# Optimization experiments

Measured on AMD Instinct MI355X. Metric: run time of the kernel, lower is better.

The kernel has to match this reference:

```python
import jax, jax.numpy as jnp
import numpy as np

N_NODES = 4096
D_MODEL = 1024
MAX_DEPS = 8
N_CLASSES = 64


def setup_inputs() -> dict:
    key = jax.random.key(0)
    k1, k2, k3 = jax.random.split(key, 3)
    questions = jax.random.normal(k1, (N_NODES, D_MODEL), dtype=jnp.float32)
    # Padded dependency lists; every dependency index is strictly < node index,
    # so processing nodes in index order is a valid topological order.
    rng = np.random.default_rng(0)
    dep_idx = np.zeros((N_NODES, MAX_DEPS), dtype=np.int32)
    dep_mask = np.zeros((N_NODES, MAX_DEPS), dtype=np.int32)
    for i in range(1, N_NODES):
        nd = int(rng.integers(1, MAX_DEPS + 1))
        dep_idx[i, :nd] = rng.integers(0, i, size=nd)
        dep_mask[i, :nd] = 1
    W1 = jax.random.normal(k2, (D_MODEL, 2 * D_MODEL), dtype=jnp.float32) * 0.02
    b1 = jnp.zeros((D_MODEL,), dtype=jnp.float32)
    W2 = jax.random.normal(k3, (N_CLASSES, D_MODEL), dtype=jnp.float32) * 0.02
    b2 = jnp.zeros((N_CLASSES,), dtype=jnp.float32)
    return {
        "questions": questions,
        "W1": W1,
        "b1": b1,
        "W2": W2,
        "b2": b2,
        "dep_idx": jnp.asarray(dep_idx),
        "dep_mask": jnp.asarray(dep_mask),
    }


def reference(questions, W1, b1, W2, b2, dep_idx, dep_mask):
    n_nodes, d_model = questions.shape

    def step(answers, xs):
        i, q, deps, mask = xs
        ctx = answers[deps]                       # [MAX_DEPS, d_model] gather
        m = mask.astype(q.dtype)
        # masked mean; all-zero mask -> zero context (matches torch zeros branch)
        ctx_mean = (ctx * m[:, None]).sum(0) / jnp.maximum(m.sum(), 1.0)
        combined = jnp.concatenate([q, ctx_mean])  # [2*d_model]
        h = jax.nn.gelu(combined @ W1.T + b1, approximate=False)
        return answers.at[i].set(h), None

    answers0 = jnp.zeros((n_nodes, d_model), dtype=questions.dtype)
    xs = (jnp.arange(n_nodes), questions, dep_idx, dep_mask)
    answers, _ = jax.lax.scan(step, answers0, xs)
    root_answer = answers[n_nodes - 1]            # root = last node in topo order
    return root_answer @ W2.T + b2                # [n_classes] logits
```

## Files before the change

kernel.cpp:

```cpp
#include <hip/hip_runtime.h>

#define NN 4096
#define DM 1024
#define MD 8
#define NW 256
#define NCOL 4
#define NT 512
#define NWAVE (NT / 64)
#define UR 4
#define MAXL 4097

#define MI_NLEV 0
#define MI_ROOTPOS 1
#define MI_ARRIVE 8
#define MI_LO 1024
#define MI_NL 6144
#define MI_PERM 10240
#define MI_DCNT 14336
#define MI_INV 18432
#define MI_DPOS 22528

typedef __attribute__((ext_vector_type(8))) short bf16x8;
typedef __attribute__((ext_vector_type(8))) unsigned short ushort8;
typedef __attribute__((ext_vector_type(4))) float f32x4;

__device__ __forceinline__ float gelu_f(float x) {
  return 0.5f * x * (1.0f + erff(x * 0.70710678118654752440f));
}
__device__ __forceinline__ unsigned short f2bf(float x) {
  unsigned int u = __builtin_bit_cast(unsigned int, x);
  u += 0x7FFFu + ((u >> 16) & 1u);
  return (unsigned short)(u >> 16);
}
__device__ __forceinline__ float bf2f(unsigned short v) {
  return __builtin_bit_cast(float, (unsigned int)v << 16);
}

__global__ __launch_bounds__(1024) void k_cvt(
    const float* __restrict__ Q, unsigned short* __restrict__ Qb) {
  const int t = threadIdx.x;
  const size_t total = (size_t)NN * DM / 8;
  for (size_t c = (size_t)blockIdx.x * 1024 + t; c < total; c += 255 * 1024) {
    const size_t i = c * 8;
    float4 a = *(const float4*)&Q[i];
    float4 b = *(const float4*)&Q[i + 4];
    ushort8 o;
    o[0] = f2bf(a.x); o[1] = f2bf(a.y); o[2] = f2bf(a.z); o[3] = f2bf(a.w);
    o[4] = f2bf(b.x); o[5] = f2bf(b.y); o[6] = f2bf(b.z); o[7] = f2bf(b.w);
    *(ushort8*)&Qb[i] = o;
  }
}

__global__ __launch_bounds__(1024) void k_fused(
    const unsigned short* __restrict__ Qb, const float* __restrict__ W1,
    const float* __restrict__ b1, const int* __restrict__ dep_idx,
    const int* __restrict__ dep_mask, int* __restrict__ meta,
    float* __restrict__ preQ) {
  __shared__ int lvl[NN];
  __shared__ int liv[NN];
  __shared__ int cnt[2 * NN];
  __shared__ int pos[NN];
  __shared__ int wflag[2][16];
  __shared__ int s_max;
  const int t = threadIdx.x;

  if (blockIdx.x != 0) {
    if (t >= 256) return;
    const int bid = blockIdx.x - 1;
    const int wave = t >> 6, lane = t & 63;
    const int wm = wave >> 1, wn = wave & 1;
    const int m0 = (bid >> 3) * 128 + wm * 64;
    const int n0 = (bid & 7) * 128 + wn * 64;
    const int lrow = lane & 15;
    const int klo = (lane >> 4) * 8;
    f32x4 acc[4][4] = {};
    for (int k0 = 0; k0 < DM; k0 += 32) {
      bf16x8 af[4];
      #pragma unroll
      for (int f = 0; f < 4; ++f)
        af[f] = *(const bf16x8*)&Qb[(size_t)(m0 + f * 16 + lrow) * DM + k0 + klo];
      bf16x8 bfr[4];
      #pragma unroll
      for (int g = 0; g < 4; ++g) {
        const float* wsrc = &W1[(size_t)(n0 + g * 16 + lrow) * 2048 + k0 + klo];
        float4 w0 = *(const float4*)&wsrc[0];
        float4 w1 = *(const float4*)&wsrc[4];
        bf16x8 bb;
        bb[0] = (short)f2bf(w0.x); bb[1] = (short)f2bf(w0.y);
        bb[2] = (short)f2bf(w0.z); bb[3] = (short)f2bf(w0.w);
        bb[4] = (short)f2bf(w1.x); bb[5] = (short)f2bf(w1.y);
        bb[6] = (short)f2bf(w1.z); bb[7] = (short)f2bf(w1.w);
        bfr[g] = bb;
      }
      #pragma unroll
      for (int f = 0; f < 4; ++f)
        #pragma unroll
        for (int g = 0; g < 4; ++g)
          acc[f][g] = __builtin_amdgcn_mfma_f32_16x16x32_bf16(af[f], bfr[g], acc[f][g], 0, 0, 0);
    }
    float b1v[4];
    #pragma unroll
    for (int g = 0; g < 4; ++g) b1v[g] = b1[n0 + g * 16 + lrow];
    const int mrow = (lane >> 4) * 4;
    #pragma unroll
    for (int f = 0; f < 4; ++f)
      #pragma unroll
      for (int g = 0; g < 4; ++g) {
        const int n = n0 + g * 16 + lrow;
        #pragma unroll
        for (int r = 0; r < 4; ++r)
          preQ[(size_t)(m0 + f * 16 + mrow + r) * DM + n] = acc[f][g][r] + b1v[g];
      }
    return;
  }

  for (int i = t; i < NN; i += 1024) { lvl[i] = 0; liv[i] = (i == NN - 1) ? 1 : 0; }
  for (int i = t; i < 2 * NN; i += 1024) cnt[i] = 0;
  if (t == 0) s_max = 0;
  __syncthreads();

  const int wid = t >> 6;
  int par = 0;

  for (int u = 0; u < 4; ++u) {
    const int i = u * 1024 + t;
    const int4 d0 = *(const int4*)&dep_idx[i * MD];
    const int4 d1 = *(const int4*)&dep_idx[i * MD + 4];
    const int4 m0 = *(const int4*)&dep_mask[i * MD];
    const int4 m1 = *(const int4*)&dep_mask[i * MD + 4];
    int my = 0;
    for (;;) {
      int m = 0;
      if (m0.x) { int l = lvl[d0.x] + 1; m = m > l ? m : l; }
      if (m0.y) { int l = lvl[d0.y] + 1; m = m > l ? m : l; }
      if (m0.z) { int l = lvl[d0.z] + 1; m = m > l ? m : l; }
      if (m0.w) { int l = lvl[d0.w] + 1; m = m > l ? m : l; }
      if (m1.x) { int l = lvl[d1.x] + 1; m = m > l ? m : l; }
      if (m1.y) { int l = lvl[d1.y] + 1; m = m > l ? m : l; }
      if (m1.z) { int l = lvl[d1.z] + 1; m = m > l ? m : l; }
      if (m1.w) { int l = lvl[d1.w] + 1; m = m > l ? m : l; }
      bool ch = false;
      if (m > my) { my = m; lvl[i] = m; ch = true; }
      const bool anyw = (__ballot(ch) != 0);
      if ((t & 63) == 0) wflag[par][wid] = anyw ? 1 : 0;
      __syncthreads();
      int any = 0;
      #pragma unroll
      for (int w = 0; w < 16; ++w) any |= wflag[par][w];
      par ^= 1;
      if (!any) break;
    }
  }
  for (int u = 3; u >= 0; --u) {
    const int i = u * 1024 + t;
    const int4 d0 = *(const int4*)&dep_idx[i * MD];
    const int4 d1 = *(const int4*)&dep_idx[i * MD + 4];
    const int4 m0 = *(const int4*)&dep_mask[i * MD];
    const int4 m1 = *(const int4*)&dep_mask[i * MD + 4];
    for (;;) {
      bool ch = false;
      if (liv[i]) {
        if (m0.x && !liv[d0.x]) { liv[d0.x] = 1; ch = true; }
        if (m0.y && !liv[d0.y]) { liv[d0.y] = 1; ch = true; }
        if (m0.z && !liv[d0.z]) { liv[d0.z] = 1; ch = true; }
        if (m0.w && !liv[d0.w]) { liv[d0.w] = 1; ch = true; }
        if (m1.x && !liv[d1.x]) { liv[d1.x] = 1; ch = true; }
        if (m1.y && !liv[d1.y]) { liv[d1.y] = 1; ch = true; }
        if (m1.z && !liv[d1.z]) { liv[d1.z] = 1; ch = true; }
        if (m1.w && !liv[d1.w]) { liv[d1.w] = 1; ch = true; }
      }
      const bool anyw = (__ballot(ch) != 0);
      if ((t & 63) == 0) wflag[par][wid] = anyw ? 1 : 0;
      __syncthreads();
      int any = 0;
      #pragma unroll
      for (int w = 0; w < 16; ++w) any |= wflag[par][w];
      par ^= 1;
      if (!any) break;
    }
  }
  for (int i = t; i < NN; i += 1024) {
    atomicAdd(&cnt[2 * lvl[i] + (liv[i] ? 0 : 1)], 1);
    atomicMax(&s_max, lvl[i]);
  }
  __syncthreads();
  const int nL = s_max + 1;
  if (t == 0) {
    int off = 0;
    for (int l = 0; l < nL; ++l) {
      meta[MI_LO + l] = off;
      meta[MI_NL + l] = cnt[2 * l];
      const int a = cnt[2 * l], b = cnt[2 * l + 1];
      cnt[2 * l] = off; off += a;
      cnt[2 * l + 1] = off; off += b;
    }
    meta[MI_LO + nL] = off;
    meta[MI_NLEV] = nL;
  }
  __syncthreads();
  for (int i = t; i < NN; i += 1024)
    pos[i] = atomicAdd(&cnt[2 * lvl[i] + (liv[i] ? 0 : 1)], 1);
  __syncthreads();
  for (int i = t; i < NN; i += 1024) {
    const int r = pos[i];
    meta[MI_PERM + r] = i;
    const int4 d0 = *(const int4*)&dep_idx[i * MD];
    const int4 d1 = *(const int4*)&dep_idx[i * MD + 4];
    const int4 m0 = *(const int4*)&dep_mask[i * MD];
    const int4 m1 = *(const int4*)&dep_mask[i * MD + 4];
    const int dd[8] = {d0.x, d0.y, d0.z, d0.w, d1.x, d1.y, d1.z, d1.w};
    const int mm[8] = {m0.x, m0.y, m0.z, m0.w, m1.x, m1.y, m1.z, m1.w};
    int nd = 0;
    #pragma unroll
    for (int k = 0; k < MD; ++k)
      if (mm[k]) { meta[MI_DPOS + r * MD + nd] = pos[dd[k]]; ++nd; }
    for (int k = nd; k < MD; ++k) meta[MI_DPOS + r * MD + k] = 0;
    meta[MI_DCNT + r] = nd;
    ((float*)meta)[MI_INV + r] = nd ? 1.0f / (float)nd : 0.0f;
  }
  if (t == 0) meta[MI_ROOTPOS] = pos[NN - 1];
  for (int i = t; i < NW; i += 1024) meta[MI_ARRIVE + i] = 0;
}

__global__ __launch_bounds__(NT) void k_levels(
    const float* __restrict__ W1, const float* __restrict__ preQ,
    unsigned short* __restrict__ hPb, float4* __restrict__ gPan, int* __restrict__ meta,
    const float* __restrict__ W2, const float* __restrict__ b2, float* __restrict__ out) {
  const int tid = threadIdx.x;
  const int wb = blockIdx.x;
  const int c0 = wb * NCOL;
  const int wave = tid >> 6, lane = tid & 63;
  const int nL = meta[MI_NLEV];
  const int rootRow = meta[MI_ROOTPOS];
  __shared__ int s_lo[MAXL];
  __shared__ int s_nl[MAXL];
  __shared__ float4 preLDS[NT];
  for (int i = tid; i <= nL; i += NT) s_lo[i] = meta[MI_LO + i];
  for (int i = tid; i < nL; i += NT) s_nl[i] = meta[MI_NL + i];
  float4 wreg[NCOL][4];
  #pragma unroll
  for (int cc = 0; cc < NCOL; ++cc)
    #pragma unroll
    for (int q = 0; q < 4; ++q)
      wreg[cc][q] = *(const float4*)&W1[(size_t)(c0 + cc) * 2048 + 1024 + lane * 16 + q * 4];
  __syncthreads();
  float4* gp = gPan + (size_t)wb * NN;
  const float* invA = (const float*)&meta[MI_INV];

  for (int l = 0; l < nL; ++l) {
    const int lo = s_lo[l];
    const int nA = s_nl[l];

    for (int r = lo + tid; r < lo + nA; r += NT) {
      const int node = meta[MI_PERM + r];
      const int nd = meta[MI_DCNT + r];
      const float iv = invA[r];
      const int4 p0 = *(const int4*)&meta[MI_DPOS + r * MD];
      const int4 p1 = *(const int4*)&meta[MI_DPOS + r * MD + 4];
      const int dps[8] = {p0.x, p0.y, p0.z, p0.w, p1.x, p1.y, p1.z, p1.w};
      float sx = 0.f, sy = 0.f, sz = 0.f, sw = 0.f;
      #pragma unroll
      for (int d = 0; d < MD; ++d) {
        float4 v = gp[dps[d]];
        sx += (d < nd) ? v.x : 0.f;
        sy += (d < nd) ? v.y : 0.f;
        sz += (d < nd) ? v.z : 0.f;
        sw += (d < nd) ? v.w : 0.f;
      }
      const float4 pq = (l > 0 && r == lo + tid) ? preLDS[tid]
                                                 : *(const float4*)&preQ[(size_t)node * DM + c0];
      const unsigned short h0 = f2bf(gelu_f(pq.x + sx * iv));
      const unsigned short h1 = f2bf(gelu_f(pq.y + sy * iv));
      const unsigned short h2 = f2bf(gelu_f(pq.z + sz * iv));
      const unsigned short h3 = f2bf(gelu_f(pq.w + sw * iv));
      const unsigned long long u = (unsigned long long)h0 | ((unsigned long long)h1 << 16)
                                 | ((unsigned long long)h2 << 32) | ((unsigned long long)h3 << 48);
      __hip_atomic_store((unsigned long long*)&hPb[(size_t)r * DM + c0], u,
                         __ATOMIC_RELAXED, __HIP_MEMORY_SCOPE_AGENT);
    }
    __syncthreads();
    if (tid == 0)
      __hip_atomic_store(&meta[MI_ARRIVE + wb], l + 1, __ATOMIC_RELAXED, __HIP_MEMORY_SCOPE_AGENT);
    if (l + 1 < nL && tid < s_nl[l + 1]) {
      const int node2 = meta[MI_PERM + s_lo[l + 1] + tid];
      preLDS[tid] = *(const float4*)&preQ[(size_t)node2 * DM + c0];
    }
    if (tid < 64) {
      for (;;) {
        int m = 1 << 30;
        #pragma unroll
        for (int u = 0; u < 4; ++u) {
          int v = __hip_atomic_load(&meta[MI_ARRIVE + tid * 4 + u], __ATOMIC_RELAXED, __HIP_MEMORY_SCOPE_AGENT);
          m = v < m ? v : m;
        }
        #pragma unroll
        for (int off = 1; off < 64; off <<= 1) {
          int o = __shfl_xor(m, off);
          m = o < m ? o : m;
        }
        if (m >= l + 1) break;
        __builtin_amdgcn_s_sleep(1);
      }
    }
    __syncthreads();

    for (int base = wave * UR; base < nA; base += NWAVE * UR) {
      const int cnt = nA - base;
      ushort8 hv[UR][2];
      #pragma unroll
      for (int u = 0; u < UR; ++u) {
        const int r = lo + base + ((u < cnt) ? u : 0);
        const ushort8* h8 = (const ushort8*)&hPb[(size_t)r * DM];
        hv[u][0] = h8[lane * 2];
        hv[u][1] = h8[lane * 2 + 1];
      }
      float rr[UR][NCOL];
      #pragma unroll
      for (int u = 0; u < UR; ++u) {
        float hf[16];
        #pragma unroll
        for (int e = 0; e < 8; ++e) { hf[e] = bf2f(hv[u][0][e]); hf[8 + e] = bf2f(hv[u][1][e]); }
        #pragma unroll
        for (int cc = 0; cc < NCOL; ++cc) {
          float a = 0.f;
          #pragma unroll
          for (int q = 0; q < 4; ++q)
            a += hf[q * 4 + 0] * wreg[cc][q].x + hf[q * 4 + 1] * wreg[cc][q].y
               + hf[q * 4 + 2] * wreg[cc][q].z + hf[q * 4 + 3] * wreg[cc][q].w;
          rr[u][cc] = a;
        }
      }
      #pragma unroll
      for (int off = 1; off < 64; off <<= 1)
        #pragma unroll
        for (int u = 0; u < UR; ++u)
          #pragma unroll
          for (int cc = 0; cc < NCOL; ++cc)
            rr[u][cc] += __shfl_xor(rr[u][cc], off);
      if (lane == 0) {
        #pragma unroll
        for (int u = 0; u < UR; ++u)
          if (u < cnt) gp[lo + base + u] = make_float4(rr[u][0], rr[u][1], rr[u][2], rr[u][3]);
      }
    }
    __syncthreads();
  }

  if (wb == 0) {
    float* red = (float*)preLDS;
    const int j = tid >> 3, kc = tid & 7;
    const ushort8* h8 = (const ushort8*)&hPb[(size_t)rootRow * DM];
    const float* wr2 = W2 + (size_t)j * DM;
    float acc = 0.f;
    for (int k = kc * 128; k < kc * 128 + 128; k += 8) {
      ushort8 hv = h8[k >> 3];
      float4 wa = *(const float4*)&wr2[k];
      float4 wb4 = *(const float4*)&wr2[k + 4];
      acc += bf2f(hv[0]) * wa.x + bf2f(hv[1]) * wa.y + bf2f(hv[2]) * wa.z + bf2f(hv[3]) * wa.w
           + bf2f(hv[4]) * wb4.x + bf2f(hv[5]) * wb4.y + bf2f(hv[6]) * wb4.z + bf2f(hv[7]) * wb4.w;
    }
    red[tid] = acc;
    __syncthreads();
    if (kc == 0) {
      float s = 0.f;
      #pragma unroll
      for (int e = 0; e < 8; ++e) s += red[j * 8 + e];
      out[j] = s + b2[j];
    }
  }
}

extern "C" void kernel_launch(void* const* d_in, const int* in_sizes, int n_in,
                              void* d_out, int out_size, void* d_ws, size_t ws_size,
                              hipStream_t stream) {
  const float* Q        = (const float*)d_in[0];
  const float* W1       = (const float*)d_in[1];
  const float* b1       = (const float*)d_in[2];
  const float* W2       = (const float*)d_in[3];
  const float* b2       = (const float*)d_in[4];
  const int*   dep_idx  = (const int*)d_in[5];
  const int*   dep_mask = (const int*)d_in[6];

  char* ws = (char*)d_ws;
  float*          preQ = (float*)ws;
  unsigned short* hPb  = (unsigned short*)(ws + (16ull << 20));
  unsigned short* Qb   = (unsigned short*)(ws + (24ull << 20));
  float4*         gPan = (float4*)(ws + (32ull << 20));
  int*            meta = (int*)(ws + (48ull << 20));
  float*          out  = (float*)d_out;

  k_cvt<<<dim3(255), dim3(1024), 0, stream>>>(Q, Qb);
  k_fused<<<dim3(257), dim3(1024), 0, stream>>>(Qb, W1, b1, dep_idx, dep_mask, meta, preQ);
  k_levels<<<dim3(NW), dim3(NT), 0, stream>>>(W1, preQ, hPb, gPan, meta, W2, b2, out);
}
```

Baseline: 481.7 us.

## Fuse question bf16 conversion into GEMM and run liveness pass in a separate block

```diff
diff --git a/kernel.cpp b/kernel.cpp
--- a/kernel.cpp
+++ b/kernel.cpp
@@ -12,6 +12,7 @@
 
 #define MI_NLEV 0
 #define MI_ROOTPOS 1
+#define MI_BWFLAG 2
 #define MI_ARRIVE 8
 #define MI_LO 1024
 #define MI_NL 6144
@@ -19,6 +20,7 @@
 #define MI_DCNT 14336
 #define MI_INV 18432
 #define MI_DPOS 22528
+#define MI_LIV 55296
 
 typedef __attribute__((ext_vector_type(8))) short bf16x8;
 typedef __attribute__((ext_vector_type(8))) unsigned short ushort8;
@@ -36,37 +38,23 @@
   return __builtin_bit_cast(float, (unsigned int)v << 16);
 }
 
-__global__ __launch_bounds__(1024) void k_cvt(
-    const float* __restrict__ Q, unsigned short* __restrict__ Qb) {
-  const int t = threadIdx.x;
-  const size_t total = (size_t)NN * DM / 8;
-  for (size_t c = (size_t)blockIdx.x * 1024 + t; c < total; c += 255 * 1024) {
-    const size_t i = c * 8;
-    float4 a = *(const float4*)&Q[i];
-    float4 b = *(const float4*)&Q[i + 4];
-    ushort8 o;
-    o[0] = f2bf(a.x); o[1] = f2bf(a.y); o[2] = f2bf(a.z); o[3] = f2bf(a.w);
-    o[4] = f2bf(b.x); o[5] = f2bf(b.y); o[6] = f2bf(b.z); o[7] = f2bf(b.w);
-    *(ushort8*)&Qb[i] = o;
-  }
-}
-
 __global__ __launch_bounds__(1024) void k_fused(
-    const unsigned short* __restrict__ Qb, const float* __restrict__ W1,
+    const float* __restrict__ Q, const float* __restrict__ W1,
     const float* __restrict__ b1, const int* __restrict__ dep_idx,
     const int* __restrict__ dep_mask, int* __restrict__ meta,
     float* __restrict__ preQ) {
   __shared__ int lvl[NN];
-  __shared__ int liv[NN];
-  __shared__ int cnt[2 * NN];
+  __shared__ int livS[NN];
+  __shared__ int cnt[2048];
   __shared__ int pos[NN];
   __shared__ int wflag[2][16];
   __shared__ int s_max;
   const int t = threadIdx.x;
-
-  if (blockIdx.x != 0) {
+  const int wid = t >> 6;
+
+  if (blockIdx.x >= 2) {
     if (t >= 256) return;
-    const int bid = blockIdx.x - 1;
+    const int bid = blockIdx.x - 2;
     const int wave = t >> 6, lane = t & 63;
     const int wm = wave >> 1, wn = wave & 1;
     const int m0 = (bid >> 3) * 128 + wm * 64;
@@ -77,8 +65,17 @@
     for (int k0 = 0; k0 < DM; k0 += 32) {
       bf16x8 af[4];
       #pragma unroll
-      for (int f = 0; f < 4; ++f)
-        af[f] = *(const bf16x8*)&Qb[(size_t)(m0 + f * 16 + lrow) * DM + k0 + klo];
+      for (int f = 0; f < 4; ++f) {
+        const float* qsrc = &Q[(size_t)(m0 + f * 16 + lrow) * DM + k0 + klo];
+        float4 q0 = *(const float4*)&qsrc[0];
+        float4 q1 = *(const float4*)&qsrc[4];
+        bf16x8 aa;
+        aa[0] = (short)f2bf(q0.x); aa[1] = (short)f2bf(q0.y);
+        aa[2] = (short)f2bf(q0.z); aa[3] = (short)f2bf(q0.w);
+        aa[4] = (short)f2bf(q1.x); aa[5] = (short)f2bf(q1.y);
+        aa[6] = (short)f2bf(q1.z); aa[7] = (short)f2bf(q1.w);
+        af[f] = aa;
+      }
       bf16x8 bfr[4];
       #pragma unroll
       for (int g = 0; g < 4; ++g) {
@@ -114,14 +111,52 @@
     return;
   }
 
-  for (int i = t; i < NN; i += 1024) { lvl[i] = 0; liv[i] = (i == NN - 1) ? 1 : 0; }
-  for (int i = t; i < 2 * NN; i += 1024) cnt[i] = 0;
+  if (blockIdx.x == 1) {
+    for (int i = t; i < NN; i += 1024) livS[i] = (i == NN - 1) ? 1 : 0;
+    __syncthreads();
+    int par = 0;
+    for (int u = 3; u >= 0; --u) {
+      const int i = u * 1024 + t;
+      const int4 d0 = *(const int4*)&dep_idx[i * MD];
+      const int4 d1 = *(const int4*)&dep_idx[i * MD + 4];
+      const int4 m0 = *(const int4*)&dep_mask[i * MD];
+      const int4 m1 = *(const int4*)&dep_mask[i * MD + 4];
+      for (;;) {
+        bool ch = false;
+        if (livS[i]) {
+          if (m0.x && !livS[d0.x]) { livS[d0.x] = 1; ch = true; }
+          if (m0.y && !livS[d0.y]) { livS[d0.y] = 1; ch = true; }
+          if (m0.z && !livS[d0.z]) { livS[d0.z] = 1; ch = true; }
+          if (m0.w && !livS[d0.w]) { livS[d0.w] = 1; ch = true; }
+          if (m1.x && !livS[d1.x]) { livS[d1.x] = 1; ch = true; }
+          if (m1.y && !livS[d1.y]) { livS[d1.y] = 1; ch = true; }
+          if (m1.z && !livS[d1.z]) { livS[d1.z] = 1; ch = true; }
+          if (m1.w && !livS[d1.w]) { livS[d1.w] = 1; ch = true; }
+        }
+        const bool anyw = (__ballot(ch) != 0);
+        if ((t & 63) == 0) wflag[par][wid] = anyw ? 1 : 0;
+        __syncthreads();
+        int any = 0;
+        #pragma unroll
+        for (int w = 0; w < 16; ++w) any |= wflag[par][w];
+        par ^= 1;
+        if (!any) break;
+      }
+    }
+    for (int i = t; i < NN; i += 1024)
+      __hip_atomic_store(&meta[MI_LIV + i], livS[i], __ATOMIC_RELAXED, __HIP_MEMORY_SCOPE_AGENT);
+    __syncthreads();
+    if (t == 0)
+      __hip_atomic_store(&meta[MI_BWFLAG], 1, __ATOMIC_RELAXED, __HIP_MEMORY_SCOPE_AGENT);
+    return;
+  }
+
+  for (int i = t; i < NN; i += 1024) lvl[i] = 0;
+  for (int i = t; i < 2048; i += 1024) cnt[i] = 0;
   if (t == 0) s_max = 0;
   __syncthreads();
 
-  const int wid = t >> 6;
   int par = 0;
-
   for (int u = 0; u < 4; ++u) {
     const int i = u * 1024 + t;
     const int4 d0 = *(const int4*)&dep_idx[i * MD];
@@ -151,36 +186,18 @@
       if (!any) break;
     }
   }
-  for (int u = 3; u >= 0; --u) {
-    const int i = u * 1024 + t;
-    const int4 d0 = *(const int4*)&dep_idx[i * MD];
-    const int4 d1 = *(const int4*)&dep_idx[i * MD + 4];
-    const int4 m0 = *(const int4*)&dep_mask[i * MD];
-    const int4 m1 = *(const int4*)&dep_mask[i * MD + 4];
-    for (;;) {
-      bool ch = false;
-      if (liv[i]) {
-        if (m0.x && !liv[d0.x]) { liv[d0.x] = 1; ch = true; }
-        if (m0.y && !liv[d0.y]) { liv[d0.y] = 1; ch = true; }
-        if (m0.z && !liv[d0.z]) { liv[d0.z] = 1; ch = true; }
-        if (m0.w && !liv[d0.w]) { liv[d0.w] = 1; ch = true; }
-        if (m1.x && !liv[d1.x]) { liv[d1.x] = 1; ch = true; }
-        if (m1.y && !liv[d1.y]) { liv[d1.y] = 1; ch = true; }
-        if (m1.z && !liv[d1.z]) { liv[d1.z] = 1; ch = true; }
-        if (m1.w && !liv[d1.w]) { liv[d1.w] = 1; ch = true; }
-      }
-      const bool anyw = (__ballot(ch) != 0);
-      if ((t & 63) == 0) wflag[par][wid] = anyw ? 1 : 0;
-      __syncthreads();
-      int any = 0;
-      #pragma unroll
-      for (int w = 0; w < 16; ++w) any |= wflag[par][w];
-      par ^= 1;
-      if (!any) break;
-    }
-  }
+
+  if (t == 0) {
+    while (__hip_atomic_load(&meta[MI_BWFLAG], __ATOMIC_RELAXED, __HIP_MEMORY_SCOPE_AGENT) != 1)
+      __builtin_amdgcn_s_sleep(8);
+  }
+  __syncthreads();
+  for (int i = t; i < NN; i += 1024)
+    livS[i] = __hip_atomic_load(&meta[MI_LIV + i], __ATOMIC_RELAXED, __HIP_MEMORY_SCOPE_AGENT);
+  __syncthreads();
+
   for (int i = t; i < NN; i += 1024) {
-    atomicAdd(&cnt[2 * lvl[i] + (liv[i] ? 0 : 1)], 1);
+    atomicAdd(&cnt[2 * lvl[i] + (livS[i] ? 0 : 1)], 1);
     atomicMax(&s_max, lvl[i]);
   }
   __syncthreads();
@@ -199,7 +216,7 @@
   }
   __syncthreads();
   for (int i = t; i < NN; i += 1024)
-    pos[i] = atomicAdd(&cnt[2 * lvl[i] + (liv[i] ? 0 : 1)], 1);
+    pos[i] = atomicAdd(&cnt[2 * lvl[i] + (livS[i] ? 0 : 1)], 1);
   __syncthreads();
   for (int i = t; i < NN; i += 1024) {
     const int r = pos[i];
@@ -305,11 +322,11 @@
     __syncthreads();
 
     for (int base = wave * UR; base < nA; base += NWAVE * UR) {
-      const int cnt = nA - base;
+      const int cnt2 = nA - base;
       ushort8 hv[UR][2];
       #pragma unroll
       for (int u = 0; u < UR; ++u) {
-        const int r = lo + base + ((u < cnt) ? u : 0);
+        const int r = lo + base + ((u < cnt2) ? u : 0);
         const ushort8* h8 = (const ushort8*)&hPb[(size_t)r * DM];
         hv[u][0] = h8[lane * 2];
         hv[u][1] = h8[lane * 2 + 1];
@@ -340,7 +357,7 @@
       if (lane == 0) {
         #pragma unroll
         for (int u = 0; u < UR; ++u)
-          if (u < cnt) gp[lo + base + u] = make_float4(rr[u][0], rr[u][1], rr[u][2], rr[u][3]);
+          if (u < cnt2) gp[lo + base + u] = make_float4(rr[u][0], rr[u][1], rr[u][2], rr[u][3]);
       }
     }
     __syncthreads();
@@ -384,12 +401,10 @@
   char* ws = (char*)d_ws;
   float*          preQ = (float*)ws;
   unsigned short* hPb  = (unsigned short*)(ws + (16ull << 20));
-  unsigned short* Qb   = (unsigned short*)(ws + (24ull << 20));
   float4*         gPan = (float4*)(ws + (32ull << 20));
   int*            meta = (int*)(ws + (48ull << 20));
   float*          out  = (float*)d_out;
 
-  k_cvt<<<dim3(255), dim3(1024), 0, stream>>>(Q, Qb);
-  k_fused<<<dim3(257), dim3(1024), 0, stream>>>(Qb, W1, b1, dep_idx, dep_mask, meta, preQ);
+  k_fused<<<dim3(258), dim3(1024), 0, stream>>>(Q, W1, b1, dep_idx, dep_mask, meta, preQ);
   k_levels<<<dim3(NW), dim3(NT), 0, stream>>>(W1, preQ, hPb, gPan, meta, W2, b2, out);
 }
```

Result: slower. 523.7 us (+8.7%).
